# Kernel tuning notes

Measured on AMD Instinct MI355X. Metric: run time of the kernel, lower is better.

The kernel has to match this reference:

```python
import jax, jax.numpy as jnp
import numpy as np

LEAKY = 0.1
NSAMPLE = 16


def _gather_group(p, idx):
    # p: [B, N, C], idx: [B, S, K] -> [B, S, K, C]
    return jax.vmap(lambda pb, ib: pb[ib])(p, idx)


def _knn_idx(x, k):
    # x: [B, N, 3]; squared pairwise distances, smallest-k indices
    sq = jnp.sum(x * x, axis=-1)  # [B, N]
    d = sq[:, :, None] + sq[:, None, :] - 2.0 * jnp.einsum('bnc,bmc->bnm', x, x)
    _, idx = jax.lax.top_k(-d, k)  # [B, N, K]
    return idx


def setup_inputs() -> dict:
    key = jax.random.key(0)
    k1, k2, k3, k4, k5 = jax.random.split(key, 5)
    B, N, D = 4, 8192, 32
    m0, m1, m2 = 32, 32, 64
    xyz = jax.random.normal(k1, (B, 3, N), dtype=jnp.float32)
    points = jax.random.normal(k2, (B, D, N), dtype=jnp.float32)
    # Conv2d 1x1 weights (kernel dims squeezed): [out, in]
    W0 = jax.random.normal(k3, (m0, D + 3), dtype=jnp.float32) * (1.0 / np.sqrt(D + 3))
    W1 = jax.random.normal(k4, (m1, m0), dtype=jnp.float32) * (1.0 / np.sqrt(m0))
    W2 = jax.random.normal(k5, (m2, m1), dtype=jnp.float32) * (1.0 / np.sqrt(m1))
    return {'xyz': xyz, 'points': points, 'W0': W0, 'W1': W1, 'W2': W2}


def reference(xyz, points, W0, W1, W2):
    lrelu = lambda x: jax.nn.leaky_relu(x, LEAKY)
    xyz_t = jnp.swapaxes(xyz, 1, 2)  # [B, N, 3]
    # pre-transform point features with feature part of first conv weight
    feat = jnp.einsum('oc,bcn->bno', W0[:, 3:], points)  # [B, N, m0]
    idx = _knn_idx(xyz_t, NSAMPLE)  # [B, N, K]
    grouped_xyz = _gather_group(xyz_t, idx)              # [B, N, K, 3]
    grouped_norm = grouped_xyz - xyz_t[:, :, None, :]    # relative coords
    grouped_feat = _gather_group(feat, idx)              # [B, N, K, m0]
    # first conv: xyz-part applied to relative coords + already-transformed feats
    x = jnp.einsum('oc,bnkc->bonk', W0[:, :3], grouped_norm) \
        + jnp.transpose(grouped_feat, (0, 3, 1, 2))      # [B, m0, N, K]
    x = lrelu(x)
    x = lrelu(jnp.einsum('oc,bcnk->bonk', W1, x))        # [B, m1, N, K]
    x = lrelu(jnp.einsum('oc,bcnk->bonk', W2, x))        # [B, m2, N, K]
    return jnp.max(x, axis=-1)                           # [B, m2, N]
```

## Files before the change

kernel.cpp:

```cpp
#include <hip/hip_runtime.h>

#define NP   8192
#define BB   4
#define DIN  32
#define M0   32
#define M1   32
#define M2   64
#define CAP  80
#define CSTR 81
#define KWV  16
#define SEG  (NP / KWV)

typedef float f32x2 __attribute__((ext_vector_type(2)));
typedef float f32x4 __attribute__((ext_vector_type(4)));
typedef short bf16x8 __attribute__((ext_vector_type(8)));

__device__ __forceinline__ float lrelu(float x) { return fmaxf(x, 0.1f * x); }
__device__ __forceinline__ unsigned umin_(unsigned a, unsigned b) { return a < b ? a : b; }
__device__ __forceinline__ unsigned umax_(unsigned a, unsigned b) { return a > b ? a : b; }

__device__ __forceinline__ unsigned fkey(float f) {
    unsigned b = __float_as_uint(f);
    return (b & 0x80000000u) ? ~b : (b | 0x80000000u);
}
__device__ __forceinline__ float funkey(unsigned k) {
    unsigned b = (k & 0x80000000u) ? (k & 0x7fffffffu) : ~k;
    return __uint_as_float(b);
}

__device__ __forceinline__ unsigned bf16rn(float f) {
    unsigned u = __float_as_uint(f);
    unsigned r = (u >> 16) & 1u;
    return (u + 0x7fffu + r) >> 16;
}

__device__ __forceinline__ f32x2 pk_fma(f32x2 a, f32x2 b, f32x2 c) {
    f32x2 d;
    asm("v_pk_fma_f32 %0, %1, %2, %3" : "=v"(d) : "v"(a), "s"(b), "v"(c));
    return d;
}

template<int CTRL>
__device__ __forceinline__ float fmax_dpp(float v) {
    int s = __builtin_amdgcn_update_dpp(0, __float_as_int(v), CTRL, 0xf, 0xf, true);
    return fmaxf(v, __int_as_float(s));
}

__device__ __forceinline__ void split_pack2(float f0, float f1, unsigned& hp, unsigned& lp) {
    unsigned u0 = __float_as_uint(f0), u1 = __float_as_uint(f1);
    unsigned h0 = u0 & 0xffff0000u, h1 = u1 & 0xffff0000u;
    hp = (u0 >> 16) | h1;
    float r0 = f0 - __uint_as_float(h0);
    float r1 = f1 - __uint_as_float(h1);
    lp = (__float_as_uint(r0) >> 16) | (__float_as_uint(r1) & 0xffff0000u);
}

__device__ __forceinline__ void wfrag(const float* wrow, bf16x8& h, bf16x8& lo) {
    float4 a = *(const float4*)(wrow);
    float4 b = *(const float4*)(wrow + 4);
    unsigned* hv = (unsigned*)&h;
    unsigned* lv = (unsigned*)&lo;
    split_pack2(a.x, a.y, hv[0], lv[0]);
    split_pack2(a.z, a.w, hv[1], lv[1]);
    split_pack2(b.x, b.y, hv[2], lv[2]);
    split_pack2(b.z, b.w, hv[3], lv[3]);
}

__device__ __forceinline__ f32x4 mfma16(bf16x8 a, bf16x8 b, f32x4 c) {
    return __builtin_amdgcn_mfma_f32_16x16x32_bf16(a, b, c, 0, 0, 0);
}

__global__ __launch_bounds__(256) void prep_kernel(
    const float* __restrict__ xyz, const float* __restrict__ points,
    const float* __restrict__ W0, float4* __restrict__ pts4,
    float4* __restrict__ ptsS, unsigned* __restrict__ featb)
{
    const int tid  = threadIdx.x;
    const int w    = __builtin_amdgcn_readfirstlane(tid >> 6);
    const int lane = tid & 63;
    const int t    = blockIdx.x * 64 + lane;
    const int b    = t >> 13;
    const int n    = t & (NP - 1);

    if (w == 0) {
        const float* xb = xyz + (size_t)b * 3 * NP;
        float x = xb[n], y = xb[NP + n], z = xb[2 * NP + n];
        float s = x * x + y * y + z * z;
        pts4[t] = make_float4(x, y, z, s);
        ptsS[t] = make_float4(-2.f * x, -2.f * y, -2.f * z, s);
    }

    const float* pb = points + (size_t)b * DIN * NP + n;
    float p[DIN];
#pragma unroll
    for (int c = 0; c < DIN; ++c) p[c] = pb[c * NP];

    uint4 outv;
    unsigned* ov = (unsigned*)&outv;
#pragma unroll
    for (int r = 0; r < 4; ++r) {
        int oe = w * 8 + 2 * r;
        float a0 = 0.f, a1 = 0.f;
#pragma unroll
        for (int c = 0; c < DIN; ++c) {
            a0 = fmaf(W0[oe * 35 + 3 + c], p[c], a0);
            a1 = fmaf(W0[(oe + 1) * 35 + 3 + c], p[c], a1);
        }
        ov[r] = bf16rn(a0) | (bf16rn(a1) << 16);
    }
    *(uint4*)(featb + (size_t)t * 16 + w * 4) = outv;
}

__global__ __launch_bounds__(1024, 8) void knn_kernel(const float4* __restrict__ pts4,
                                                      const float4* __restrict__ ptsS,
                                                      int* __restrict__ idxout)
{
    __shared__ unsigned skey[64 * 65];
    __shared__ float    sT[64];
    __shared__ int      scnt[64];
    __shared__ float    cand_t[64 * CSTR];
    __shared__ int      cand_i[64 * CSTR];

    const int tid  = threadIdx.x;
    const int w    = __builtin_amdgcn_readfirstlane(tid >> 6);
    const int lane = tid & 63;
    const int blk  = blockIdx.x;
    const int b    = blk >> 7;
    const int n0   = (blk & 127) << 6;
    const int bn0  = b * NP;
    const float4* P  = pts4 + bn0;
    const float4* S  = ptsS + bn0;
    const float4* Pq = P + n0;

    for (int i = tid; i < 64 * 65; i += 1024) skey[i] = 0xFFFFFFFFu;
    if (tid < 64) scnt[tid] = 0;
    __syncthreads();

    const int base = w * SEG;
    f32x2 sx[4], sy[4], sz[4], sw2[4];
#pragma unroll
    for (int jp = 0; jp < 4; ++jp) {
        float4 a = S[base + (2 * jp) * 64 + lane];
        float4 c = S[base + (2 * jp + 1) * 64 + lane];
        sx[jp].x = a.x;  sx[jp].y = c.x;
        sy[jp].x = a.y;  sy[jp].y = c.y;
        sz[jp].x = a.z;  sz[jp].y = c.z;
        sw2[jp].x = a.w; sw2[jp].y = c.w;
    }

    float4 qnxt[8];
#pragma unroll
    for (int i = 0; i < 8; ++i) qnxt[i] = Pq[i];
#pragma unroll 1
    for (int qc = 0; qc < 8; ++qc) {
        float4 qv[8];
#pragma unroll
        for (int i = 0; i < 8; ++i) qv[i] = qnxt[i];
        if (qc < 7) {
#pragma unroll
            for (int i = 0; i < 8; ++i) qnxt[i] = Pq[(qc + 1) * 8 + i];
        }
#pragma unroll
        for (int i = 0; i < 8; ++i) {
            f32x2 qx, qy, qz;
            qx.x = qv[i].x; qx.y = qv[i].x;
            qy.x = qv[i].y; qy.y = qv[i].y;
            qz.x = qv[i].z; qz.y = qv[i].z;
            f32x2 t0 = pk_fma(sz[0], qz, sw2[0]);
            f32x2 t1 = pk_fma(sz[1], qz, sw2[1]);
            f32x2 t2 = pk_fma(sz[2], qz, sw2[2]);
            f32x2 t3 = pk_fma(sz[3], qz, sw2[3]);
            t0 = pk_fma(sy[0], qy, t0);  t1 = pk_fma(sy[1], qy, t1);
            t2 = pk_fma(sy[2], qy, t2);  t3 = pk_fma(sy[3], qy, t3);
            t0 = pk_fma(sx[0], qx, t0);  t1 = pk_fma(sx[1], qx, t1);
            t2 = pk_fma(sx[2], qx, t2);  t3 = pk_fma(sx[3], qx, t3);
            float a  = fminf(fminf(t0.x, t0.y), t1.x);
            float b2 = fminf(fminf(t1.y, t2.x), t2.y);
            float c2 = fminf(fminf(t3.x, t3.y), a);
            float mn = fminf(b2, c2);
            atomicMin(&skey[(qc * 8 + i) * 65 + lane], fkey(mn));
        }
    }
    __syncthreads();

    if (tid < 64) {
        unsigned t16[16];
#pragma unroll
        for (int i = 0; i < 16; ++i) t16[i] = 0xFFFFFFFFu;
        for (int c = 0; c < 64; ++c) {
            unsigned d = skey[tid * 65 + c];
            if (d < t16[15]) {
                t16[15] = d;
#pragma unroll
                for (int i = 15; i > 0; --i) {
                    unsigned a = t16[i - 1], cc = t16[i];
                    t16[i - 1] = umin_(a, cc);
                    t16[i]     = umax_(a, cc);
                }
            }
        }
        sT[tid] = funkey(t16[15]);
    }
    __syncthreads();

#pragma unroll
    for (int i = 0; i < 8; ++i) qnxt[i] = Pq[i];
#pragma unroll 1
    for (int qc = 0; qc < 8; ++qc) {
        float4 qv[8];
#pragma unroll
        for (int i = 0; i < 8; ++i) qv[i] = qnxt[i];
        if (qc < 7) {
#pragma unroll
            for (int i = 0; i < 8; ++i) qnxt[i] = Pq[(qc + 1) * 8 + i];
        }
#pragma unroll
        for (int i = 0; i < 8; ++i) {
            const int q = qc * 8 + i;
            const float T = sT[q];
            f32x2 qx, qy, qz;
            qx.x = qv[i].x; qx.y = qv[i].x;
            qy.x = qv[i].y; qy.y = qv[i].y;
            qz.x = qv[i].z; qz.y = qv[i].z;
#pragma unroll
            for (int jp = 0; jp < 4; ++jp) {
                f32x2 t = pk_fma(sz[jp], qz, sw2[jp]);
                t = pk_fma(sy[jp], qy, t);
                t = pk_fma(sx[jp], qx, t);
                if (t.x <= T) {
                    int pos = atomicAdd(&scnt[q], 1);
                    if (pos < CAP) {
                        cand_t[q * CSTR + pos] = t.x;
                        cand_i[q * CSTR + pos] = base + (2 * jp) * 64 + lane;
                    }
                }
                if (t.y <= T) {
                    int pos = atomicAdd(&scnt[q], 1);
                    if (pos < CAP) {
                        cand_t[q * CSTR + pos] = t.y;
                        cand_i[q * CSTR + pos] = base + (2 * jp + 1) * 64 + lane;
                    }
                }
            }
        }
    }
    __syncthreads();

    if (tid < 64) {
        int cnt = scnt[tid];
        int* outp = idxout + ((bn0 + n0 + tid) << 4);
        float bd[16]; int bi[16];
#pragma unroll
        for (int i = 0; i < 16; ++i) { bd[i] = 3e38f; bi[i] = 0; }
        if (cnt <= CAP) {
            for (int pos = 0; pos < cnt; ++pos) {
                float d = cand_t[tid * CSTR + pos];
                int   j = cand_i[tid * CSTR + pos];
                if ((d < bd[15]) || (d == bd[15] && j < bi[15])) {
                    bd[15] = d; bi[15] = j;
#pragma unroll
                    for (int i = 15; i > 0; --i) {
                        bool sw = (bd[i] < bd[i - 1]) || (bd[i] == bd[i - 1] && bi[i] < bi[i - 1]);
                        float td = bd[i - 1]; int tj = bi[i - 1];
                        bd[i - 1] = sw ? bd[i] : td;  bi[i - 1] = sw ? bi[i] : tj;
                        bd[i]     = sw ? td : bd[i];  bi[i]     = sw ? tj : bi[i];
                    }
                }
            }
        } else {
            float4 q4 = Pq[tid];
            for (int j = 0; j < NP; ++j) {
                float4 s = S[j];
                float d = fmaf(q4.x, s.x, fmaf(q4.y, s.y, fmaf(q4.z, s.z, s.w)));
                if ((d < bd[15]) || (d == bd[15] && j < bi[15])) {
                    bd[15] = d; bi[15] = j;
#pragma unroll
                    for (int i = 15; i > 0; --i) {
                        bool sw = (bd[i] < bd[i - 1]) || (bd[i] == bd[i - 1] && bi[i] < bi[i - 1]);
                        float td = bd[i - 1]; int tj = bi[i - 1];
                        bd[i - 1] = sw ? bd[i] : td;  bi[i - 1] = sw ? bi[i] : tj;
                        bd[i]     = sw ? td : bd[i];  bi[i]     = sw ? tj : bi[i];
                    }
                }
            }
        }
#pragma unroll
        for (int i = 0; i < 16; ++i) outp[i] = bi[i];
    }
}

__global__ __launch_bounds__(256, 4) void conv_kernel(
    const float4* __restrict__ pts4, const unsigned* __restrict__ featb,
    const int* __restrict__ idx,
    const float* __restrict__ W0, const float* __restrict__ W1, const float* __restrict__ W2,
    float* __restrict__ out)
{
    __shared__ __align__(16) unsigned short sh_hi[4][4][64][8];
    __shared__ __align__(16) unsigned short sh_lo[4][4][64][8];
    __shared__ float so[M2][17];

    const int tid = threadIdx.x;
    const int w   = __builtin_amdgcn_readfirstlane(tid >> 6);
    const int l   = tid & 63;
    const int g   = l >> 4;
    const int q   = l & 15;
    const int k   = tid & 15;
    const int nl  = tid >> 4;
    const int blk = blockIdx.x;
    const int b   = blk >> 9;
    const int n0  = (blk & 511) << 4;
    const int n   = n0 + nl;
    const int bn  = b * NP + n;
    const int j   = idx[(bn << 4) + k];
    const int bj  = b * NP + j;

    const float4 pc = pts4[bn];
    const float4 pj = pts4[bj];
    const float rx = pj.x - pc.x, ry = pj.y - pc.y, rz = pj.z - pc.z;

    const uint4* fj = (const uint4*)(featb + (size_t)bj * 16);

#pragma unroll
    for (int gg = 0; gg < 4; ++gg) {
        uint4 u = fj[gg];
        const unsigned* uv = (const unsigned*)&u;
        uint4 hv, lv;
        unsigned* hp = (unsigned*)&hv;
        unsigned* lp = (unsigned*)&lv;
#pragma unroll
        for (int r = 0; r < 4; ++r) {
            int o = gg * 8 + 2 * r;
            float fe  = __uint_as_float(uv[r] << 16);
            float fo_ = __uint_as_float(uv[r] & 0xffff0000u);
            float e0 = lrelu(fmaf(W0[o * 35], rx, fmaf(W0[o * 35 + 1], ry, fmaf(W0[o * 35 + 2], rz, fe))));
            float e1 = lrelu(fmaf(W0[(o + 1) * 35], rx, fmaf(W0[(o + 1) * 35 + 1], ry, fmaf(W0[(o + 1) * 35 + 2], rz, fo_))));
            split_pack2(e0, e1, hp[r], lp[r]);
        }
        *(uint4*)&sh_hi[w][gg][l][0] = hv;
        *(uint4*)&sh_lo[w][gg][l][0] = lv;
    }

    bf16x8 b1h[4], b1l[4];
#pragma unroll
    for (int t = 0; t < 4; ++t) {
        b1h[t] = *(const bf16x8*)&sh_hi[w][g][16 * t + q][0];
        b1l[t] = *(const bf16x8*)&sh_lo[w][g][16 * t + q][0];
    }
    const f32x4 zz = {0.f, 0.f, 0.f, 0.f};
#pragma unroll
    for (int r = 0; r < 2; ++r) {
        bf16x8 wh, wl;
        wfrag(W1 + (16 * r + q) * 32 + g * 8, wh, wl);
#pragma unroll
        for (int t = 0; t < 4; ++t) {
            f32x4 a = mfma16(wl, b1h[t], zz);
            a = mfma16(wh, b1l[t], a);
            a = mfma16(wh, b1h[t], a);
            float v0 = lrelu(a[0]);
            float v1 = lrelu(a[1]);
            float v2 = lrelu(a[2]);
            float v3 = lrelu(a[3]);
            uint2 hv, lv;
            split_pack2(v0, v1, hv.x, lv.x);
            split_pack2(v2, v3, hv.y, lv.y);
            const int kg = 2 * r + (g >> 1);
            const int ko = 4 * (g & 1);
            *(uint2*)&sh_hi[w][kg][16 * t + q][ko] = hv;
            *(uint2*)&sh_lo[w][kg][16 * t + q][ko] = lv;
        }
    }

    bf16x8 b2h[4], b2l[4];
#pragma unroll
    for (int t = 0; t < 4; ++t) {
        b2h[t] = *(const bf16x8*)&sh_hi[w][g][16 * t + q][0];
        b2l[t] = *(const bf16x8*)&sh_lo[w][g][16 * t + q][0];
    }
#pragma unroll
    for (int rr = 0; rr < 4; ++rr) {
        bf16x8 wh, wl;
        wfrag(W2 + (16 * rr + q) * 32 + g * 8, wh, wl);
#pragma unroll
        for (int t = 0; t < 4; ++t) {
            f32x4 a = mfma16(wl, b2h[t], zz);
            a = mfma16(wh, b2l[t], a);
            a = mfma16(wh, b2h[t], a);
#pragma unroll
            for (int reg = 0; reg < 4; ++reg) {
                float v = lrelu(a[reg]);
                v = fmax_dpp<0xB1>(v);
                v = fmax_dpp<0x4E>(v);
                v = fmax_dpp<0x141>(v);
                v = fmax_dpp<0x140>(v);
                if (q == reg) so[16 * rr + 4 * g + reg][w * 4 + t] = v;
            }
        }
    }
    __syncthreads();
    {
        int o = tid >> 2;
        int col = (tid & 3) << 2;
        float4 v = make_float4(so[o][col], so[o][col + 1], so[o][col + 2], so[o][col + 3]);
        *(float4*)(out + ((size_t)(b * M2 + o)) * NP + n0 + col) = v;
    }
}

extern "C" void kernel_launch(void* const* d_in, const int* in_sizes, int n_in,
                              void* d_out, int out_size, void* d_ws, size_t ws_size,
                              hipStream_t stream)
{
    const float* xyz    = (const float*)d_in[0];
    const float* points = (const float*)d_in[1];
    const float* W0     = (const float*)d_in[2];
    const float* W1     = (const float*)d_in[3];
    const float* W2     = (const float*)d_in[4];
    float* out = (float*)d_out;

    char* ws = (char*)d_ws;
    float4*   pts4  = (float4*)ws;
    float4*   ptsS  = (float4*)(ws + 0x080000);
    unsigned* featb = (unsigned*)(ws + 0x100000);
    int*      idx   = (int*)(ws + 0x300000);

    prep_kernel<<<BB * NP / 64, 256,  0, stream>>>(xyz, points, W0, pts4, ptsS, featb);
    knn_kernel <<<BB * NP / 64, 1024, 0, stream>>>(pts4, ptsS, idx);
    conv_kernel<<<BB * NP / 16, 256,  0, stream>>>(pts4, featb, idx, W0, W1, W2, out);
}
```

Before: 208.5 us.

## Shrink KNN blocks to 32 queries, precompute weight fragments, swap max reduction

The KNN kernel now handles 32 queries per 512-thread block, and each wave scans two 512-point segments. Blocks are smaller and twice as many, which may raise occupancy and shrink shared memory per block. W1 and W2 are split into bf16 hi/lo MFMA fragments once in the prep kernel and loaded precomputed in the conv kernel, so each block no longer rebuilds them. The final max over K swaps the MFMA operand order, so it becomes an in-register max plus a swizzle and a shuffle, replacing four DPP steps per register, and applies leaky ReLU after the max (valid because leaky ReLU is monotonic).

```diff
diff --git a/kernel.cpp b/kernel.cpp
--- a/kernel.cpp
+++ b/kernel.cpp
@@ -8,8 +8,7 @@
 #define M2   64
 #define CAP  80
 #define CSTR 81
-#define KWV  16
-#define SEG  (NP / KWV)
+#define KQ   32
 
 typedef float f32x2 __attribute__((ext_vector_type(2)));
 typedef float f32x4 __attribute__((ext_vector_type(4)));
@@ -38,12 +37,6 @@
     f32x2 d;
     asm("v_pk_fma_f32 %0, %1, %2, %3" : "=v"(d) : "v"(a), "s"(b), "v"(c));
     return d;
-}
-
-template<int CTRL>
-__device__ __forceinline__ float fmax_dpp(float v) {
-    int s = __builtin_amdgcn_update_dpp(0, __float_as_int(v), CTRL, 0xf, 0xf, true);
-    return fmaxf(v, __int_as_float(s));
 }
 
 __device__ __forceinline__ void split_pack2(float f0, float f1, unsigned& hp, unsigned& lp) {
@@ -72,8 +65,10 @@
 
 __global__ __launch_bounds__(256) void prep_kernel(
     const float* __restrict__ xyz, const float* __restrict__ points,
-    const float* __restrict__ W0, float4* __restrict__ pts4,
-    float4* __restrict__ ptsS, unsigned* __restrict__ featb)
+    const float* __restrict__ W0, const float* __restrict__ W1,
+    const float* __restrict__ W2, float4* __restrict__ pts4,
+    float4* __restrict__ ptsS, unsigned* __restrict__ featb,
+    uint4* __restrict__ w1f, uint4* __restrict__ w2f)
 {
     const int tid  = threadIdx.x;
     const int w    = __builtin_amdgcn_readfirstlane(tid >> 6);
@@ -109,81 +104,95 @@
         ov[r] = bf16rn(a0) | (bf16rn(a1) << 16);
     }
     *(uint4*)(featb + (size_t)t * 16 + w * 4) = outv;
-}
-
-__global__ __launch_bounds__(1024, 8) void knn_kernel(const float4* __restrict__ pts4,
-                                                      const float4* __restrict__ ptsS,
-                                                      int* __restrict__ idxout)
+
+    if (blockIdx.x == 0 && tid < 64) {
+        const int qq = tid & 15, gg = tid >> 4;
+        bf16x8 h, lo;
+#pragma unroll
+        for (int r = 0; r < 2; ++r) {
+            wfrag(W1 + (16 * r + qq) * 32 + gg * 8, h, lo);
+            w1f[(r * 64 + tid) * 2 + 0] = *(uint4*)&h;
+            w1f[(r * 64 + tid) * 2 + 1] = *(uint4*)&lo;
+        }
+#pragma unroll
+        for (int rr = 0; rr < 4; ++rr) {
+            wfrag(W2 + (16 * rr + qq) * 32 + gg * 8, h, lo);
+            w2f[(rr * 64 + tid) * 2 + 0] = *(uint4*)&h;
+            w2f[(rr * 64 + tid) * 2 + 1] = *(uint4*)&lo;
+        }
+    }
+}
+
+__global__ __launch_bounds__(512, 8) void knn_kernel(const float4* __restrict__ pts4,
+                                                     const float4* __restrict__ ptsS,
+                                                     int* __restrict__ idxout)
 {
-    __shared__ unsigned skey[64 * 65];
-    __shared__ float    sT[64];
-    __shared__ int      scnt[64];
-    __shared__ float    cand_t[64 * CSTR];
-    __shared__ int      cand_i[64 * CSTR];
+    __shared__ unsigned skey[KQ * 65];
+    __shared__ float    sT[KQ];
+    __shared__ int      scnt[KQ];
+    __shared__ float    cand_t[KQ * CSTR];
+    __shared__ int      cand_i[KQ * CSTR];
 
     const int tid  = threadIdx.x;
     const int w    = __builtin_amdgcn_readfirstlane(tid >> 6);
     const int lane = tid & 63;
     const int blk  = blockIdx.x;
-    const int b    = blk >> 7;
-    const int n0   = (blk & 127) << 6;
+    const int b    = blk >> 8;
+    const int n0   = (blk & 255) << 5;
     const int bn0  = b * NP;
     const float4* P  = pts4 + bn0;
     const float4* S  = ptsS + bn0;
     const float4* Pq = P + n0;
 
-    for (int i = tid; i < 64 * 65; i += 1024) skey[i] = 0xFFFFFFFFu;
-    if (tid < 64) scnt[tid] = 0;
+    for (int i = tid; i < KQ * 65; i += 512) skey[i] = 0xFFFFFFFFu;
+    if (tid < KQ) scnt[tid] = 0;
     __syncthreads();
 
-    const int base = w * SEG;
-    f32x2 sx[4], sy[4], sz[4], sw2[4];
-#pragma unroll
-    for (int jp = 0; jp < 4; ++jp) {
-        float4 a = S[base + (2 * jp) * 64 + lane];
-        float4 c = S[base + (2 * jp + 1) * 64 + lane];
-        sx[jp].x = a.x;  sx[jp].y = c.x;
-        sy[jp].x = a.y;  sy[jp].y = c.y;
-        sz[jp].x = a.z;  sz[jp].y = c.z;
-        sw2[jp].x = a.w; sw2[jp].y = c.w;
-    }
-
-    float4 qnxt[8];
-#pragma unroll
-    for (int i = 0; i < 8; ++i) qnxt[i] = Pq[i];
+    const int base = w * 1024;
+
 #pragma unroll 1
-    for (int qc = 0; qc < 8; ++qc) {
-        float4 qv[8];
-#pragma unroll
-        for (int i = 0; i < 8; ++i) qv[i] = qnxt[i];
-        if (qc < 7) {
-#pragma unroll
-            for (int i = 0; i < 8; ++i) qnxt[i] = Pq[(qc + 1) * 8 + i];
-        }
-#pragma unroll
-        for (int i = 0; i < 8; ++i) {
-            f32x2 qx, qy, qz;
-            qx.x = qv[i].x; qx.y = qv[i].x;
-            qy.x = qv[i].y; qy.y = qv[i].y;
-            qz.x = qv[i].z; qz.y = qv[i].z;
-            f32x2 t0 = pk_fma(sz[0], qz, sw2[0]);
-            f32x2 t1 = pk_fma(sz[1], qz, sw2[1]);
-            f32x2 t2 = pk_fma(sz[2], qz, sw2[2]);
-            f32x2 t3 = pk_fma(sz[3], qz, sw2[3]);
-            t0 = pk_fma(sy[0], qy, t0);  t1 = pk_fma(sy[1], qy, t1);
-            t2 = pk_fma(sy[2], qy, t2);  t3 = pk_fma(sy[3], qy, t3);
-            t0 = pk_fma(sx[0], qx, t0);  t1 = pk_fma(sx[1], qx, t1);
-            t2 = pk_fma(sx[2], qx, t2);  t3 = pk_fma(sx[3], qx, t3);
-            float a  = fminf(fminf(t0.x, t0.y), t1.x);
-            float b2 = fminf(fminf(t1.y, t2.x), t2.y);
-            float c2 = fminf(fminf(t3.x, t3.y), a);
-            float mn = fminf(b2, c2);
-            atomicMin(&skey[(qc * 8 + i) * 65 + lane], fkey(mn));
+    for (int sg = 0; sg < 2; ++sg) {
+        const int sb = base + sg * 512;
+        f32x2 sx[4], sy[4], sz[4], sw2[4];
+#pragma unroll
+        for (int jp = 0; jp < 4; ++jp) {
+            float4 a = S[sb + (2 * jp) * 64 + lane];
+            float4 c = S[sb + (2 * jp + 1) * 64 + lane];
+            sx[jp].x = a.x;  sx[jp].y = c.x;
+            sy[jp].x = a.y;  sy[jp].y = c.y;
+            sz[jp].x = a.z;  sz[jp].y = c.z;
+            sw2[jp].x = a.w; sw2[jp].y = c.w;
+        }
+#pragma unroll 1
+        for (int qc = 0; qc < 4; ++qc) {
+            float4 qv[8];
+#pragma unroll
+            for (int i = 0; i < 8; ++i) qv[i] = Pq[qc * 8 + i];
+#pragma unroll
+            for (int i = 0; i < 8; ++i) {
+                f32x2 qx, qy, qz;
+                qx.x = qv[i].x; qx.y = qv[i].x;
+                qy.x = qv[i].y; qy.y = qv[i].y;
+                qz.x = qv[i].z; qz.y = qv[i].z;
+                f32x2 t0 = pk_fma(sz[0], qz, sw2[0]);
+                f32x2 t1 = pk_fma(sz[1], qz, sw2[1]);
+                f32x2 t2 = pk_fma(sz[2], qz, sw2[2]);
+                f32x2 t3 = pk_fma(sz[3], qz, sw2[3]);
+                t0 = pk_fma(sy[0], qy, t0);  t1 = pk_fma(sy[1], qy, t1);
+                t2 = pk_fma(sy[2], qy, t2);  t3 = pk_fma(sy[3], qy, t3);
+                t0 = pk_fma(sx[0], qx, t0);  t1 = pk_fma(sx[1], qx, t1);
+                t2 = pk_fma(sx[2], qx, t2);  t3 = pk_fma(sx[3], qx, t3);
+                float a  = fminf(fminf(t0.x, t0.y), t1.x);
+                float b2 = fminf(fminf(t1.y, t2.x), t2.y);
+                float c2 = fminf(fminf(t3.x, t3.y), a);
+                float mn = fminf(b2, c2);
+                atomicMin(&skey[(qc * 8 + i) * 65 + lane], fkey(mn));
+            }
         }
     }
     __syncthreads();
 
-    if (tid < 64) {
+    if (tid < KQ) {
         unsigned t16[16];
 #pragma unroll
         for (int i = 0; i < 16; ++i) t16[i] = 0xFFFFFFFFu;
@@ -203,42 +212,50 @@
     }
     __syncthreads();
 
-#pragma unroll
-    for (int i = 0; i < 8; ++i) qnxt[i] = Pq[i];
 #pragma unroll 1
-    for (int qc = 0; qc < 8; ++qc) {
-        float4 qv[8];
-#pragma unroll
-        for (int i = 0; i < 8; ++i) qv[i] = qnxt[i];
-        if (qc < 7) {
-#pragma unroll
-            for (int i = 0; i < 8; ++i) qnxt[i] = Pq[(qc + 1) * 8 + i];
-        }
-#pragma unroll
-        for (int i = 0; i < 8; ++i) {
-            const int q = qc * 8 + i;
-            const float T = sT[q];
-            f32x2 qx, qy, qz;
-            qx.x = qv[i].x; qx.y = qv[i].x;
-            qy.x = qv[i].y; qy.y = qv[i].y;
-            qz.x = qv[i].z; qz.y = qv[i].z;
-#pragma unroll
-            for (int jp = 0; jp < 4; ++jp) {
-                f32x2 t = pk_fma(sz[jp], qz, sw2[jp]);
-                t = pk_fma(sy[jp], qy, t);
-                t = pk_fma(sx[jp], qx, t);
-                if (t.x <= T) {
-                    int pos = atomicAdd(&scnt[q], 1);
-                    if (pos < CAP) {
-                        cand_t[q * CSTR + pos] = t.x;
-                        cand_i[q * CSTR + pos] = base + (2 * jp) * 64 + lane;
+    for (int sg = 0; sg < 2; ++sg) {
+        const int sb = base + sg * 512;
+        f32x2 sx[4], sy[4], sz[4], sw2[4];
+#pragma unroll
+        for (int jp = 0; jp < 4; ++jp) {
+            float4 a = S[sb + (2 * jp) * 64 + lane];
+            float4 c = S[sb + (2 * jp + 1) * 64 + lane];
+            sx[jp].x = a.x;  sx[jp].y = c.x;
+            sy[jp].x = a.y;  sy[jp].y = c.y;
+            sz[jp].x = a.z;  sz[jp].y = c.z;
+            sw2[jp].x = a.w; sw2[jp].y = c.w;
+        }
+#pragma unroll 1
+        for (int qc = 0; qc < 4; ++qc) {
+            float4 qv[8];
+#pragma unroll
+            for (int i = 0; i < 8; ++i) qv[i] = Pq[qc * 8 + i];
+#pragma unroll
+            for (int i = 0; i < 8; ++i) {
+                const int q = qc * 8 + i;
+                const float T = sT[q];
+                f32x2 qx, qy, qz;
+                qx.x = qv[i].x; qx.y = qv[i].x;
+                qy.x = qv[i].y; qy.y = qv[i].y;
+                qz.x = qv[i].z; qz.y = qv[i].z;
+#pragma unroll
+                for (int jp = 0; jp < 4; ++jp) {
+                    f32x2 t = pk_fma(sz[jp], qz, sw2[jp]);
+                    t = pk_fma(sy[jp], qy, t);
+                    t = pk_fma(sx[jp], qx, t);
+                    if (t.x <= T) {
+                        int pos = atomicAdd(&scnt[q], 1);
+                        if (pos < CAP) {
+                            cand_t[q * CSTR + pos] = t.x;
+                            cand_i[q * CSTR + pos] = sb + (2 * jp) * 64 + lane;
+                        }
                     }
-                }
-                if (t.y <= T) {
-                    int pos = atomicAdd(&scnt[q], 1);
-                    if (pos < CAP) {
-                        cand_t[q * CSTR + pos] = t.y;
-                        cand_i[q * CSTR + pos] = base + (2 * jp + 1) * 64 + lane;
+                    if (t.y <= T) {
+                        int pos = atomicAdd(&scnt[q], 1);
+                        if (pos < CAP) {
+                            cand_t[q * CSTR + pos] = t.y;
+                            cand_i[q * CSTR + pos] = sb + (2 * jp + 1) * 64 + lane;
+                        }
                     }
                 }
             }
@@ -246,7 +263,7 @@
     }
     __syncthreads();
 
-    if (tid < 64) {
+    if (tid < KQ) {
         int cnt = scnt[tid];
         int* outp = idxout + ((bn0 + n0 + tid) << 4);
         float bd[16]; int bi[16];
@@ -291,8 +308,8 @@
 
 __global__ __launch_bounds__(256, 4) void conv_kernel(
     const float4* __restrict__ pts4, const unsigned* __restrict__ featb,
-    const int* __restrict__ idx,
-    const float* __restrict__ W0, const float* __restrict__ W1, const float* __restrict__ W2,
+    const int* __restrict__ idx, const float* __restrict__ W0,
+    const uint4* __restrict__ w1f, const uint4* __restrict__ w2f,
     float* __restrict__ out)
 {
     __shared__ __align__(16) unsigned short sh_hi[4][4][64][8];
@@ -349,8 +366,8 @@
     const f32x4 zz = {0.f, 0.f, 0.f, 0.f};
 #pragma unroll
     for (int r = 0; r < 2; ++r) {
-        bf16x8 wh, wl;
-        wfrag(W1 + (16 * r + q) * 32 + g * 8, wh, wl);
+        bf16x8 wh = *(const bf16x8*)&w1f[(r * 64 + l) * 2 + 0];
+        bf16x8 wl = *(const bf16x8*)&w1f[(r * 64 + l) * 2 + 1];
 #pragma unroll
         for (int t = 0; t < 4; ++t) {
             f32x4 a = mfma16(wl, b1h[t], zz);
@@ -378,22 +395,17 @@
     }
 #pragma unroll
     for (int rr = 0; rr < 4; ++rr) {
-        bf16x8 wh, wl;
-        wfrag(W2 + (16 * rr + q) * 32 + g * 8, wh, wl);
+        bf16x8 wh = *(const bf16x8*)&w2f[(rr * 64 + l) * 2 + 0];
+        bf16x8 wl = *(const bf16x8*)&w2f[(rr * 64 + l) * 2 + 1];
 #pragma unroll
         for (int t = 0; t < 4; ++t) {
-            f32x4 a = mfma16(wl, b2h[t], zz);
-            a = mfma16(wh, b2l[t], a);
-            a = mfma16(wh, b2h[t], a);
-#pragma unroll
-            for (int reg = 0; reg < 4; ++reg) {
-                float v = lrelu(a[reg]);
-                v = fmax_dpp<0xB1>(v);
-                v = fmax_dpp<0x4E>(v);
-                v = fmax_dpp<0x141>(v);
-                v = fmax_dpp<0x140>(v);
-                if (q == reg) so[16 * rr + 4 * g + reg][w * 4 + t] = v;
-            }
+            f32x4 a = mfma16(b2h[t], wl, zz);
+            a = mfma16(b2l[t], wh, a);
+            a = mfma16(b2h[t], wh, a);
+            float m = fmaxf(fmaxf(a[0], a[1]), fmaxf(a[2], a[3]));
+            m = fmaxf(m, __int_as_float(__builtin_amdgcn_ds_swizzle(__float_as_int(m), 0x401F)));
+            m = fmaxf(m, __shfl_xor(m, 32));
+            if (g == 0) so[16 * rr + q][w * 4 + t] = lrelu(m);
         }
     }
     __syncthreads();
@@ -421,8 +433,10 @@
     float4*   ptsS  = (float4*)(ws + 0x080000);
     unsigned* featb = (unsigned*)(ws + 0x100000);
     int*      idx   = (int*)(ws + 0x300000);
-
-    prep_kernel<<<BB * NP / 64, 256,  0, stream>>>(xyz, points, W0, pts4, ptsS, featb);
-    knn_kernel <<<BB * NP / 64, 1024, 0, stream>>>(pts4, ptsS, idx);
-    conv_kernel<<<BB * NP / 16, 256,  0, stream>>>(pts4, featb, idx, W0, W1, W2, out);
-}
+    uint4*    w1f   = (uint4*)(ws + 0x500000);
+    uint4*    w2f   = (uint4*)(ws + 0x502000);
+
+    prep_kernel<<<BB * NP / 64, 256,  0, stream>>>(xyz, points, W0, W1, W2, pts4, ptsS, featb, w1f, w2f);
+    knn_kernel <<<BB * NP / KQ, 512,  0, stream>>>(pts4, ptsS, idx);
+    conv_kernel<<<BB * NP / 16, 256,  0, stream>>>(pts4, featb, idx, W0, w1f, w2f, out);
+}
```

After: 185.4 us. 1.12x faster.
